# Optimization experiments

Hardware: AMD Instinct MI355X
Metric: run time of the kernel (lower is better)

Reference implementation:

```python
import jax, jax.numpy as jnp
import numpy as np

KH, KW = 3, 3
STRIDE = 1
PADDING = 1
CIN, COUT = 64, 64


def setup_inputs() -> dict:
    key = jax.random.key(0)
    kx, kw, kb = jax.random.split(key, 3)
    x = jax.random.normal(kx, (16, CIN, 112, 112), dtype=jnp.float32)
    # Kaiming-uniform style init, matching the torch module
    fan = CIN * KH * KW
    gain = np.sqrt(2.0)
    bound_w = np.sqrt(3.0) * gain / np.sqrt(fan)
    weights = jax.random.uniform(kw, (COUT, CIN, KH, KW), dtype=jnp.float32,
                                 minval=-bound_w, maxval=bound_w)
    bound_b = 1.0 / np.sqrt(fan)
    bias = jax.random.uniform(kb, (COUT,), dtype=jnp.float32,
                              minval=-bound_b, maxval=bound_b)
    return {"x": x, "weights": weights, "bias": bias}


def reference(x, weights, bias):
    # Equivalent to F.unfold + GEMM: a standard cross-correlation conv.
    # x: (N, C, H, W), weights: (F, C, KH, KW) -> out: (N, F, H', W')
    out = jax.lax.conv_general_dilated(
        x, weights,
        window_strides=(STRIDE, STRIDE),
        padding=((PADDING, PADDING), (PADDING, PADDING)),
        dimension_numbers=("NCHW", "OIHW", "NCHW"),
    )
    return out + bias[None, :, None, None]
```

## Files before the change

### kernel.cpp

```cpp
#include <hip/hip_runtime.h>


typedef __attribute__((ext_vector_type(8))) short bf16x8;
typedef __attribute__((ext_vector_type(4))) float f32x4;

#define CIN 64
#define COUT 64
#define HH 112
#define WW 112
#define ROWS 2
#define TILES 7
#define STRIPH (ROWS * TILES)
#define NPL 8
#define WPITCH 67
#define PLANE_SHORTS (8 * WPITCH * 8)
#define LDS_SHORTS (NPL * PLANE_SHORTS)

__device__ __forceinline__ int ladr(int pl, int oct, int w) {
    return ((pl * 8 + oct) * WPITCH + w) * 8;
}

__device__ __forceinline__ unsigned short f2bf(float f) {
    unsigned u = __builtin_bit_cast(unsigned, f);
    u += 0x7FFFu + ((u >> 16) & 1u);
    return (unsigned short)(u >> 16);
}

#if __has_builtin(__builtin_amdgcn_cvt_pk_bf16_f32)
__device__ __forceinline__ unsigned pk2bf(float a, float b) {
    typedef __attribute__((ext_vector_type(2))) __bf16 bf16x2;
    bf16x2 r = __builtin_amdgcn_cvt_pk_bf16_f32(a, b);
    return __builtin_bit_cast(unsigned, r);
}
#else
__device__ __forceinline__ unsigned pk2bf(float a, float b) {
    return (unsigned)f2bf(a) | ((unsigned)f2bf(b) << 16);
}
#endif

__global__ void conv_wprep(const float* __restrict__ w, short* __restrict__ wbf) {
    int i = blockIdx.x * 256 + threadIdx.x;
    int j = i & 7;
    int f = (i >> 3) & 63;
    int koct = (i >> 9) & 3;
    int cb = (i >> 11) & 1;
    int t = i >> 12;
    int c = cb * 32 + koct * 8 + j;
    int ky = t / 3, kx = t - ky * 3;
    wbf[i] = (short)f2bf(w[((f * CIN + c) * 3 + ky) * 3 + kx]);
}

struct StageRegs {
    float4 v[8];
    float hv;
};

__device__ __forceinline__ void stage_load(const float* __restrict__ x, int tid,
                                           int n, int c0, int W4N, int gce,
                                           int row0, StageRegs& sr)
{
    if (tid < 256) {
        const int re = tid >> 7, oct = (tid >> 4) & 7, w4 = tid & 15;
        const int row = row0 + re;
#pragma unroll
        for (int k = 0; k < 8; ++k) sr.v[k] = (float4){0.f, 0.f, 0.f, 0.f};
        if ((unsigned)row < (unsigned)HH && w4 < W4N) {
            const float* px = x + (((n * CIN + oct * 8) * HH + row) * WW + c0 + w4 * 4);
#pragma unroll
            for (int k = 0; k < 8; ++k) sr.v[k] = *(const float4*)(px + k * HH * WW);
        }
    } else if (tid < 384) {
        const int i = tid - 256;
        const int row = row0 + (i >> 6);
        sr.hv = 0.f;
        if ((unsigned)row < (unsigned)HH)
            sr.hv = x[((n * CIN + (i & 63)) * HH + row) * WW + gce];
    }
}

__device__ __forceinline__ void stage_write(short* lds, int tid, int W4N,
                                            int padw, int wedge, int row0,
                                            const StageRegs& sr)
{
    if (tid < 256) {
        const int re = tid >> 7, oct = (tid >> 4) & 7, w4 = tid & 15;
        const int pl = (row0 + re) & (NPL - 1);
        if (w4 < W4N) {
            const float* fv = (const float*)&sr.v[0];
#pragma unroll
            for (int dw = 0; dw < 4; ++dw) {
                uint4 pk;
                pk.x = pk2bf(fv[0 * 4 + dw], fv[1 * 4 + dw]);
                pk.y = pk2bf(fv[2 * 4 + dw], fv[3 * 4 + dw]);
                pk.z = pk2bf(fv[4 * 4 + dw], fv[5 * 4 + dw]);
                pk.w = pk2bf(fv[6 * 4 + dw], fv[7 * 4 + dw]);
                *(uint4*)&lds[ladr(pl, oct, 1 + w4 * 4 + dw)] = pk;
            }
        }
    } else if (tid < 384) {
        const int i = tid - 256;
        const int row = row0 + (i >> 6);
        const int pl = row & (NPL - 1);
        const int c = i & 63;
        lds[ladr(pl, c >> 3, wedge) + (c & 7)] = (short)f2bf(sr.hv);
    } else if (tid < 400) {
        const int i = tid - 384;
        const int pl = (row0 + (i >> 3)) & (NPL - 1);
        *(uint4*)&lds[ladr(pl, i & 7, padw)] = (uint4){0u, 0u, 0u, 0u};
    }
}

__global__ __launch_bounds__(512, 2)
void conv3x3_mfma(const float* __restrict__ x, const short* __restrict__ wbf,
                  const float* __restrict__ bias, float* __restrict__ out)
{
    __shared__ __align__(16) short lds[LDS_SHORTS];
    const int tid = threadIdx.x;
    const int n = blockIdx.x;
    const int ws = blockIdx.y;
    const int hb = blockIdx.z * STRIPH;

    const int MTN   = ws ? 3 : 4;
    const int W4N   = ws ? 12 : 16;
    const int c0    = ws * 64;
    const int padw  = ws ? 49 : 0;
    const int gce   = ws ? 63 : 64;
    const int wedge = ws ? 0 : 65;

    const int wave = tid >> 6;
    const int r  = wave >> 2;
    const int nh = (wave >> 1) & 1;
    const int mh = wave & 1;
    const int lane = tid & 63;
    const int lm = lane & 15;
    const int q  = lane >> 4;

    StageRegs sr;

    stage_load(x, tid, n, c0, W4N, gce, hb - 1, sr);
    stage_write(lds, tid, W4N, padw, wedge, hb - 1, sr);
    stage_load(x, tid, n, c0, W4N, gce, hb + 1, sr);
    stage_write(lds, tid, W4N, padw, wedge, hb + 1, sr);

    bf16x8 bw[9][2][2];
#pragma unroll
    for (int t = 0; t < 9; ++t)
#pragma unroll
        for (int ntl = 0; ntl < 2; ++ntl) {
            const int f = nh * 32 + ntl * 16 + lm;
            bw[t][ntl][0] = *(const bf16x8*)(wbf + (t * 8 + q) * 512 + f * 8);
            bw[t][ntl][1] = *(const bf16x8*)(wbf + (t * 8 + 4 + q) * 512 + f * 8);
        }

    const int f0 = nh * 32 + lm;
    const float b0 = bias[f0];
    const float b1 = bias[f0 + 16];

    __syncthreads();

    for (int t = 0; t < TILES; ++t) {
        const int h0 = hb + 2 * t;
        const bool do_stage = (t < TILES - 1);

        if (do_stage) stage_load(x, tid, n, c0, W4N, gce, h0 + 3, sr);

        f32x4 acc[2][2];
#pragma unroll
        for (int j = 0; j < 2; ++j)
#pragma unroll
            for (int ntl = 0; ntl < 2; ++ntl) acc[j][ntl] = (f32x4){0.f, 0.f, 0.f, 0.f};

#pragma unroll
        for (int tap = 0; tap < 9; ++tap) {
            const int ky = tap / 3, kx = tap - ky * 3;
            const int pl = (h0 - 1 + r + ky) & (NPL - 1);
#pragma unroll
            for (int j = 0; j < 2; ++j) {
                const int mt = mh * 2 + j;
                if (mt < MTN) {
                    const int wcol = mt * 16 + lm + kx;
                    const bf16x8 a0 = *(const bf16x8*)&lds[ladr(pl, q, wcol)];
                    const bf16x8 a1 = *(const bf16x8*)&lds[ladr(pl, q + 4, wcol)];
                    acc[j][0] = __builtin_amdgcn_mfma_f32_16x16x32_bf16(a0, bw[tap][0][0], acc[j][0], 0, 0, 0);
                    acc[j][1] = __builtin_amdgcn_mfma_f32_16x16x32_bf16(a0, bw[tap][1][0], acc[j][1], 0, 0, 0);
                    acc[j][0] = __builtin_amdgcn_mfma_f32_16x16x32_bf16(a1, bw[tap][0][1], acc[j][0], 0, 0, 0);
                    acc[j][1] = __builtin_amdgcn_mfma_f32_16x16x32_bf16(a1, bw[tap][1][1], acc[j][1], 0, 0, 0);
                }
            }
        }

        if (do_stage) stage_write(lds, tid, W4N, padw, wedge, h0 + 3, sr);

        const int hrow = h0 + r;
#pragma unroll
        for (int j = 0; j < 2; ++j) {
            const int mt = mh * 2 + j;
            if (mt < MTN) {
#pragma unroll
                for (int ntl = 0; ntl < 2; ++ntl) {
                    const f32x4 v = acc[j][ntl];
                    const float bb = ntl ? b1 : b0;
                    float4 s;
                    s.x = v[0] + bb; s.y = v[1] + bb; s.z = v[2] + bb; s.w = v[3] + bb;
                    *(float4*)(out + ((n * COUT + f0 + ntl * 16) * HH + hrow) * WW
                               + c0 + mt * 16 + q * 4) = s;
                }
            }
        }

        __syncthreads();
    }
}

extern "C" void kernel_launch(void* const* d_in, const int* in_sizes, int n_in,
                              void* d_out, int out_size, void* d_ws, size_t ws_size,
                              hipStream_t stream) {
    const float* x = (const float*)d_in[0];
    const float* w = (const float*)d_in[1];
    const float* b = (const float*)d_in[2];
    float* out = (float*)d_out;
    short* wbf = (short*)d_ws;

    conv_wprep<<<144, 256, 0, stream>>>(w, wbf);
    dim3 grid(16, 2, 8);
    conv3x3_mfma<<<grid, 512, 0, stream>>>(x, wbf, b, out);
}
```

Baseline: 115.7 us.

## Stage four rows per barrier with ten-plane LDS ring and fewer syncs

The LDS row ring grows from 8 to 10 planes and staging now loads up to four input rows per step using all 512 threads. Two 2-row output tiles are computed per barrier, which roughly halves the number of block barriers and lets global loads overlap more compute. Barriers become lgkmcnt waits plus s_barrier wrapped in sched_barriers, and weight registers are pinned with empty asm. The cost is more LDS per block, which may reduce occupancy, plus modulo-10 plane indexing instead of a mask and more registers held live.

```diff
diff --git a/kernel.cpp b/kernel.cpp
--- a/kernel.cpp
+++ b/kernel.cpp
@@ -8,13 +8,12 @@
 #define COUT 64
 #define HH 112
 #define WW 112
-#define ROWS 2
-#define TILES 7
-#define STRIPH (ROWS * TILES)
-#define NPL 8
+#define NPL 10
 #define WPITCH 67
 #define PLANE_SHORTS (8 * WPITCH * 8)
 #define LDS_SHORTS (NPL * PLANE_SHORTS)
+
+__device__ __forceinline__ int pmod(int row) { return (row + NPL) % NPL; }
 
 __device__ __forceinline__ int ladr(int pl, int oct, int w) {
     return ((pl * 8 + oct) * WPITCH + w) * 8;
@@ -37,6 +36,13 @@
     return (unsigned)f2bf(a) | ((unsigned)f2bf(b) << 16);
 }
 #endif
+
+#define BAR_LGKM() do {                                   \
+    __builtin_amdgcn_sched_barrier(0);                    \
+    asm volatile("s_waitcnt lgkmcnt(0)" ::: "memory");    \
+    __builtin_amdgcn_s_barrier();                         \
+    __builtin_amdgcn_sched_barrier(0);                    \
+} while (0)
 
 __global__ void conv_wprep(const float* __restrict__ w, short* __restrict__ wbf) {
     int i = blockIdx.x * 256 + threadIdx.x;
@@ -57,56 +63,108 @@
 
 __device__ __forceinline__ void stage_load(const float* __restrict__ x, int tid,
                                            int n, int c0, int W4N, int gce,
-                                           int row0, StageRegs& sr)
-{
-    if (tid < 256) {
-        const int re = tid >> 7, oct = (tid >> 4) & 7, w4 = tid & 15;
-        const int row = row0 + re;
-#pragma unroll
-        for (int k = 0; k < 8; ++k) sr.v[k] = (float4){0.f, 0.f, 0.f, 0.f};
-        if ((unsigned)row < (unsigned)HH && w4 < W4N) {
-            const float* px = x + (((n * CIN + oct * 8) * HH + row) * WW + c0 + w4 * 4);
-#pragma unroll
-            for (int k = 0; k < 8; ++k) sr.v[k] = *(const float4*)(px + k * HH * WW);
-        }
-    } else if (tid < 384) {
-        const int i = tid - 256;
-        const int row = row0 + (i >> 6);
-        sr.hv = 0.f;
-        if ((unsigned)row < (unsigned)HH)
-            sr.hv = x[((n * CIN + (i & 63)) * HH + row) * WW + gce];
-    }
+                                           int row0, int nr, StageRegs& sr)
+{
+    const int re  = tid >> 7;
+    const int oct = (tid >> 4) & 7;
+    const int w4  = tid & 15;
+    const int row = row0 + re;
+#pragma unroll
+    for (int k = 0; k < 8; ++k) sr.v[k] = (float4){0.f, 0.f, 0.f, 0.f};
+    sr.hv = 0.f;
+    if (re < nr && (unsigned)row < (unsigned)HH && w4 < W4N) {
+        const float* px = x + (((n * CIN + oct * 8) * HH + row) * WW + c0 + w4 * 4);
+#pragma unroll
+        for (int k = 0; k < 8; ++k) sr.v[k] = *(const float4*)(px + k * HH * WW);
+    }
+    const int hr = tid >> 6;
+    const int hrow = row0 + hr;
+    if (hr < nr && (unsigned)hrow < (unsigned)HH)
+        sr.hv = x[((n * CIN + (tid & 63)) * HH + hrow) * WW + gce];
 }
 
 __device__ __forceinline__ void stage_write(short* lds, int tid, int W4N,
                                             int padw, int wedge, int row0,
-                                            const StageRegs& sr)
-{
-    if (tid < 256) {
-        const int re = tid >> 7, oct = (tid >> 4) & 7, w4 = tid & 15;
-        const int pl = (row0 + re) & (NPL - 1);
-        if (w4 < W4N) {
-            const float* fv = (const float*)&sr.v[0];
-#pragma unroll
-            for (int dw = 0; dw < 4; ++dw) {
-                uint4 pk;
-                pk.x = pk2bf(fv[0 * 4 + dw], fv[1 * 4 + dw]);
-                pk.y = pk2bf(fv[2 * 4 + dw], fv[3 * 4 + dw]);
-                pk.z = pk2bf(fv[4 * 4 + dw], fv[5 * 4 + dw]);
-                pk.w = pk2bf(fv[6 * 4 + dw], fv[7 * 4 + dw]);
-                *(uint4*)&lds[ladr(pl, oct, 1 + w4 * 4 + dw)] = pk;
+                                            int nr, const StageRegs& sr)
+{
+    const int re  = tid >> 7;
+    const int oct = (tid >> 4) & 7;
+    const int w4  = tid & 15;
+    if (re < nr && w4 < W4N) {
+        const int pl = pmod(row0 + re);
+        const float* fv = (const float*)&sr.v[0];
+#pragma unroll
+        for (int dw = 0; dw < 4; ++dw) {
+            uint4 pk;
+            pk.x = pk2bf(fv[0 * 4 + dw], fv[1 * 4 + dw]);
+            pk.y = pk2bf(fv[2 * 4 + dw], fv[3 * 4 + dw]);
+            pk.z = pk2bf(fv[4 * 4 + dw], fv[5 * 4 + dw]);
+            pk.w = pk2bf(fv[6 * 4 + dw], fv[7 * 4 + dw]);
+            *(uint4*)&lds[ladr(pl, oct, 1 + w4 * 4 + dw)] = pk;
+        }
+    }
+    const int hr = tid >> 6;
+    if (hr < nr) {
+        const int pl = pmod(row0 + hr);
+        const int c = tid & 63;
+        lds[ladr(pl, c >> 3, wedge) + (c & 7)] = (short)f2bf(sr.hv);
+    }
+    if (tid < 8 * nr) {
+        const int pl = pmod(row0 + (tid >> 3));
+        *(uint4*)&lds[ladr(pl, tid & 7, padw)] = (uint4){0u, 0u, 0u, 0u};
+    }
+}
+
+__device__ __forceinline__ void tile_compute(const short* lds,
+    const bf16x8 (&bw)[9][2][2], float* __restrict__ out,
+    int n, int c0, int MTN, int h0, int r, int nh, int mh, int lm, int q,
+    float b0, float b1)
+{
+    f32x4 acc[2][2];
+#pragma unroll
+    for (int j = 0; j < 2; ++j)
+#pragma unroll
+        for (int ntl = 0; ntl < 2; ++ntl) acc[j][ntl] = (f32x4){0.f, 0.f, 0.f, 0.f};
+
+    const int hro = h0 - 1 + r;
+    int pls[3];
+    pls[0] = pmod(hro); pls[1] = pmod(hro + 1); pls[2] = pmod(hro + 2);
+
+#pragma unroll
+    for (int tap = 0; tap < 9; ++tap) {
+        const int ky = tap / 3, kx = tap - ky * 3;
+        const int pl = pls[ky];
+#pragma unroll
+        for (int j = 0; j < 2; ++j) {
+            const int mt = mh * 2 + j;
+            if (mt < MTN) {
+                const int wcol = mt * 16 + lm + kx;
+                const bf16x8 a0 = *(const bf16x8*)&lds[ladr(pl, q, wcol)];
+                const bf16x8 a1 = *(const bf16x8*)&lds[ladr(pl, q + 4, wcol)];
+                acc[j][0] = __builtin_amdgcn_mfma_f32_16x16x32_bf16(a0, bw[tap][0][0], acc[j][0], 0, 0, 0);
+                acc[j][1] = __builtin_amdgcn_mfma_f32_16x16x32_bf16(a0, bw[tap][1][0], acc[j][1], 0, 0, 0);
+                acc[j][0] = __builtin_amdgcn_mfma_f32_16x16x32_bf16(a1, bw[tap][0][1], acc[j][0], 0, 0, 0);
+                acc[j][1] = __builtin_amdgcn_mfma_f32_16x16x32_bf16(a1, bw[tap][1][1], acc[j][1], 0, 0, 0);
             }
         }
-    } else if (tid < 384) {
-        const int i = tid - 256;
-        const int row = row0 + (i >> 6);
-        const int pl = row & (NPL - 1);
-        const int c = i & 63;
-        lds[ladr(pl, c >> 3, wedge) + (c & 7)] = (short)f2bf(sr.hv);
-    } else if (tid < 400) {
-        const int i = tid - 384;
-        const int pl = (row0 + (i >> 3)) & (NPL - 1);
-        *(uint4*)&lds[ladr(pl, i & 7, padw)] = (uint4){0u, 0u, 0u, 0u};
+    }
+
+    const int f0 = nh * 32 + lm;
+    const int hrow = h0 + r;
+#pragma unroll
+    for (int j = 0; j < 2; ++j) {
+        const int mt = mh * 2 + j;
+        if (mt < MTN) {
+#pragma unroll
+            for (int ntl = 0; ntl < 2; ++ntl) {
+                const f32x4 v = acc[j][ntl];
+                const float bb = ntl ? b1 : b0;
+                float4 s;
+                s.x = v[0] + bb; s.y = v[1] + bb; s.z = v[2] + bb; s.w = v[3] + bb;
+                *(float4*)(out + ((n * COUT + f0 + ntl * 16) * HH + hrow) * WW
+                           + c0 + mt * 16 + q * 4) = s;
+            }
+        }
     }
 }
 
@@ -118,7 +176,7 @@
     const int tid = threadIdx.x;
     const int n = blockIdx.x;
     const int ws = blockIdx.y;
-    const int hb = blockIdx.z * STRIPH;
+    const int hb = blockIdx.z * 14;
 
     const int MTN   = ws ? 3 : 4;
     const int W4N   = ws ? 12 : 16;
@@ -137,10 +195,11 @@
 
     StageRegs sr;
 
-    stage_load(x, tid, n, c0, W4N, gce, hb - 1, sr);
-    stage_write(lds, tid, W4N, padw, wedge, hb - 1, sr);
-    stage_load(x, tid, n, c0, W4N, gce, hb + 1, sr);
-    stage_write(lds, tid, W4N, padw, wedge, hb + 1, sr);
+    stage_load (x,  tid, n, c0, W4N, gce,  hb - 1, 4, sr);
+    stage_write(lds, tid, W4N, padw, wedge, hb - 1, 4, sr);
+    stage_load (x,  tid, n, c0, W4N, gce,  hb + 3, 2, sr);
+    stage_write(lds, tid, W4N, padw, wedge, hb + 3, 2, sr);
+    stage_load (x,  tid, n, c0, W4N, gce,  hb + 5, 4, sr);
 
     bf16x8 bw[9][2][2];
 #pragma unroll
@@ -151,65 +210,31 @@
             bw[t][ntl][0] = *(const bf16x8*)(wbf + (t * 8 + q) * 512 + f * 8);
             bw[t][ntl][1] = *(const bf16x8*)(wbf + (t * 8 + 4 + q) * 512 + f * 8);
         }
+#pragma unroll
+    for (int t = 0; t < 9; ++t)
+#pragma unroll
+        for (int ntl = 0; ntl < 2; ++ntl)
+#pragma unroll
+            for (int cb = 0; cb < 2; ++cb)
+                asm volatile("" : "=v"(bw[t][ntl][cb]) : "0"(bw[t][ntl][cb]));
 
     const int f0 = nh * 32 + lm;
     const float b0 = bias[f0];
     const float b1 = bias[f0 + 16];
 
-    __syncthreads();
-
-    for (int t = 0; t < TILES; ++t) {
-        const int h0 = hb + 2 * t;
-        const bool do_stage = (t < TILES - 1);
-
-        if (do_stage) stage_load(x, tid, n, c0, W4N, gce, h0 + 3, sr);
-
-        f32x4 acc[2][2];
-#pragma unroll
-        for (int j = 0; j < 2; ++j)
-#pragma unroll
-            for (int ntl = 0; ntl < 2; ++ntl) acc[j][ntl] = (f32x4){0.f, 0.f, 0.f, 0.f};
-
-#pragma unroll
-        for (int tap = 0; tap < 9; ++tap) {
-            const int ky = tap / 3, kx = tap - ky * 3;
-            const int pl = (h0 - 1 + r + ky) & (NPL - 1);
-#pragma unroll
-            for (int j = 0; j < 2; ++j) {
-                const int mt = mh * 2 + j;
-                if (mt < MTN) {
-                    const int wcol = mt * 16 + lm + kx;
-                    const bf16x8 a0 = *(const bf16x8*)&lds[ladr(pl, q, wcol)];
-                    const bf16x8 a1 = *(const bf16x8*)&lds[ladr(pl, q + 4, wcol)];
-                    acc[j][0] = __builtin_amdgcn_mfma_f32_16x16x32_bf16(a0, bw[tap][0][0], acc[j][0], 0, 0, 0);
-                    acc[j][1] = __builtin_amdgcn_mfma_f32_16x16x32_bf16(a0, bw[tap][1][0], acc[j][1], 0, 0, 0);
-                    acc[j][0] = __builtin_amdgcn_mfma_f32_16x16x32_bf16(a1, bw[tap][0][1], acc[j][0], 0, 0, 0);
-                    acc[j][1] = __builtin_amdgcn_mfma_f32_16x16x32_bf16(a1, bw[tap][1][1], acc[j][1], 0, 0, 0);
-                }
-            }
-        }
-
-        if (do_stage) stage_write(lds, tid, W4N, padw, wedge, h0 + 3, sr);
-
-        const int hrow = h0 + r;
-#pragma unroll
-        for (int j = 0; j < 2; ++j) {
-            const int mt = mh * 2 + j;
-            if (mt < MTN) {
-#pragma unroll
-                for (int ntl = 0; ntl < 2; ++ntl) {
-                    const f32x4 v = acc[j][ntl];
-                    const float bb = ntl ? b1 : b0;
-                    float4 s;
-                    s.x = v[0] + bb; s.y = v[1] + bb; s.z = v[2] + bb; s.w = v[3] + bb;
-                    *(float4*)(out + ((n * COUT + f0 + ntl * 16) * HH + hrow) * WW
-                               + c0 + mt * 16 + q * 4) = s;
-                }
-            }
-        }
-
-        __syncthreads();
-    }
+    BAR_LGKM();
+
+#pragma unroll 1
+    for (int p = 0; p < 3; ++p) {
+        const int oh = hb + 4 * p;
+        tile_compute(lds, bw, out, n, c0, MTN, oh, r, nh, mh, lm, q, b0, b1);
+        stage_write(lds, tid, W4N, padw, wedge, oh + 5, (p == 2) ? 2 : 4, sr);
+        if (p == 0)      stage_load(x, tid, n, c0, W4N, gce, oh + 9, 4, sr);
+        else if (p == 1) stage_load(x, tid, n, c0, W4N, gce, oh + 9, 2, sr);
+        tile_compute(lds, bw, out, n, c0, MTN, oh + 2, r, nh, mh, lm, q, b0, b1);
+        BAR_LGKM();
+    }
+    tile_compute(lds, bw, out, n, c0, MTN, hb + 12, r, nh, mh, lm, q, b0, b1);
 }
 
 extern "C" void kernel_launch(void* const* d_in, const int* in_sizes, int n_in,
```

After: 119.4 us. 1.03x slower.
